# Kernel tuning notes

Hardware: AMD Instinct MI355X
Metric: run time of the kernel (lower is better)

Reference implementation:

```python
import jax, jax.numpy as jnp
import numpy as np

D = 64       # CNF state dimension
H = 512      # MLP hidden width
B = 8192     # batch


def setup_inputs() -> dict:
    key = jax.random.key(0)
    ks = jax.random.split(key, 8)
    s1 = 1.0 / np.sqrt(D + 1)
    s2 = 1.0 / np.sqrt(H)
    return {
        "t": jax.random.uniform(ks[0], (1,), dtype=jnp.float32),
        "x": jax.random.normal(ks[1], (B, D + 1), dtype=jnp.float32),
        "W1": jax.random.normal(ks[2], (D + 1, H), dtype=jnp.float32) * s1,
        "b1": jnp.zeros((H,), dtype=jnp.float32),
        "W2": jax.random.normal(ks[3], (H, H), dtype=jnp.float32) * s2,
        "b2": jnp.zeros((H,), dtype=jnp.float32),
        "W3": jax.random.normal(ks[4], (H, D), dtype=jnp.float32) * s2,
        "b3": jnp.zeros((D,), dtype=jnp.float32),
    }


def reference(t, x, W1, b1, W2, b2, W3, b3):
    # CNF.forward: strip log-density channel, evaluate vf and its exact divergence.
    xs = x[..., :-1]                      # [B, D]
    tt = t[0]

    def vf_single(xi):                    # xi: [D] -> [D]
        inp = jnp.concatenate([tt[None], xi])          # vf(t*ones, x) with t prepended
        h = jnp.tanh(inp @ W1 + b1)
        h = jnp.tanh(h @ W2 + b2)
        return h @ W3 + b3

    dx = jax.vmap(vf_single)(xs)                        # [B, D]
    # exact divergence: trace of per-sample Jacobian via reverse-mode (matches torch jacrev)
    J = jax.vmap(jax.jacrev(vf_single))(xs)             # [B, D, D]
    div = jnp.trace(J, axis1=-2, axis2=-1)              # [B]
    return jnp.concatenate([dx, div[:, None]], axis=-1) # [B, D+1]
```

## Files before the change

kernel.cpp:

```cpp
#include <hip/hip_runtime.h>

#define HH 512
#define DD 64
#define MROWS 32
#define TPB 1024
#define LP 520

typedef unsigned short u16;
typedef short s16x8 __attribute__((ext_vector_type(8)));
typedef float f32x4 __attribute__((ext_vector_type(4)));

#define MFMA16(A,B,C) __builtin_amdgcn_mfma_f32_16x16x32_bf16((A),(B),(C),0,0,0)

#define OFF_EF   0
#define OFF_W2F  (HH*HH)
#define OFF_W1F  (2*HH*HH)
#define OFF_W3F  (2*HH*HH + HH*DD)
#define OFF_Z0B  ((2*HH*HH + 2*HH*DD)*2)

__device__ __forceinline__ u16 f2bf(float f) {
    unsigned u = __builtin_bit_cast(unsigned, f);
    u += 0x7fffu + ((u >> 16) & 1u);
    return (u16)(u >> 16);
}
__device__ __forceinline__ float bf2f(u16 h) {
    return __builtin_bit_cast(float, (unsigned)h << 16);
}
__device__ __forceinline__ float fast_tanh(float x) {
    float e = __expf(2.0f * x);
    return 1.0f - 2.0f * __builtin_amdgcn_rcpf(e + 1.0f);
}

__global__ __launch_bounds__(256) void precompute(
    const float* __restrict__ t,  const float* __restrict__ W1,
    const float* __restrict__ b1, const float* __restrict__ W2,
    const float* __restrict__ W3, u16* __restrict__ ws16, float* __restrict__ z0)
{
    __shared__ float GL[16 * 520];
    u16* Ef  = ws16 + OFF_EF;
    u16* W2f = ws16 + OFF_W2F;
    u16* W1f = ws16 + OFF_W1F;
    u16* W3f = ws16 + OFF_W3F;

    const int bid = blockIdx.x, tid = threadIdx.x;

    if (bid < 32) {
        const int nt   = bid;
        const int a0   = nt * 16;
        const int lane = tid & 63, w = tid >> 6;
        const int m16  = lane & 15, q = lane >> 4;

        s16x8 afh[2], afl[2];
#pragma unroll
        for (int h = 0; h < 2; ++h) {
#pragma unroll
            for (int j = 0; j < 8; ++j) {
                int i = h * 32 + q * 8 + j;
                float v = W1[(1 + i) * HH + a0 + m16];
                u16 hi = f2bf(v);
                afh[h][j] = (short)hi;
                afl[h][j] = (short)f2bf(v - bf2f(hi));
            }
        }
        for (int bt = 0; bt < 8; ++bt) {
            int b0 = w * 128 + bt * 16;
            s16x8 bfh[2], bfl[2];
#pragma unroll
            for (int h = 0; h < 2; ++h) {
                const float* src = W3 + (b0 + m16) * DD + h * 32 + q * 8;
                float4 p0 = *(const float4*)(src);
                float4 p1 = *(const float4*)(src + 4);
                float vv[8] = {p0.x,p0.y,p0.z,p0.w,p1.x,p1.y,p1.z,p1.w};
#pragma unroll
                for (int j = 0; j < 8; ++j) {
                    u16 hi = f2bf(vv[j]);
                    bfh[h][j] = (short)hi;
                    bfl[h][j] = (short)f2bf(vv[j] - bf2f(hi));
                }
            }
            f32x4 c = {0.f, 0.f, 0.f, 0.f};
#pragma unroll
            for (int h = 0; h < 2; ++h) {
                c = MFMA16(afh[h], bfh[h], c);
                c = MFMA16(afh[h], bfl[h], c);
                c = MFMA16(afl[h], bfh[h], c);
            }
#pragma unroll
            for (int r = 0; r < 4; ++r)
                GL[(4 * q + r) * 520 + b0 + m16] = c[r];
        }
        __syncthreads();

        for (int p = 0; p < 4; ++p) {
            int ks = p * 4 + (tid >> 6);
            int ln = tid & 63;
            int al = ln & 15;
            int bq = ks * 32 + (ln >> 4) * 8;
            const float* w2p = W2 + (a0 + al) * HH + bq;
            const float* glp = GL + al * 520 + bq;
            float4 wa = *(const float4*)(w2p), wb = *(const float4*)(w2p + 4);
            float4 ga = *(const float4*)(glp), gb = *(const float4*)(glp + 4);
            s16x8 o;
            o[0]=(short)f2bf(wa.x*ga.x); o[1]=(short)f2bf(wa.y*ga.y);
            o[2]=(short)f2bf(wa.z*ga.z); o[3]=(short)f2bf(wa.w*ga.w);
            o[4]=(short)f2bf(wb.x*gb.x); o[5]=(short)f2bf(wb.y*gb.y);
            o[6]=(short)f2bf(wb.z*gb.z); o[7]=(short)f2bf(wb.w*gb.w);
            *(s16x8*)(Ef + nt * 8192 + ks * 512 + ln * 8) = o;
        }
        for (int p = 0; p < 4; ++p) {
            int ks = p * 4 + (tid >> 6);
            int ln = tid & 63;
            int n  = nt * 16 + (ln & 15);
            int k0 = ks * 32 + (ln >> 4) * 8;
            s16x8 o;
#pragma unroll
            for (int j = 0; j < 8; ++j) o[j] = (short)f2bf(W2[(k0 + j) * HH + n]);
            *(s16x8*)(W2f + nt * 8192 + ks * 512 + ln * 8) = o;
        }
        if (tid < 128) {
            int ks = tid >> 6, ln = tid & 63;
            int n  = nt * 16 + (ln & 15);
            int k0 = ks * 32 + (ln >> 4) * 8;
            s16x8 o;
#pragma unroll
            for (int j = 0; j < 8; ++j) o[j] = (short)f2bf(W1[(1 + k0 + j) * HH + n]);
            *(s16x8*)(W1f + nt * 1024 + ks * 512 + ln * 8) = o;
        }
    } else if (bid < 36) {
        int ot = bid - 32;
        for (int p = 0; p < 4; ++p) {
            int ks = p * 4 + (tid >> 6);
            int ln = tid & 63;
            int o  = ot * 16 + (ln & 15);
            int k0 = ks * 32 + (ln >> 4) * 8;
            s16x8 v;
#pragma unroll
            for (int j = 0; j < 8; ++j) v[j] = (short)f2bf(W3[(k0 + j) * DD + o]);
            *(s16x8*)(W3f + ot * 8192 + ks * 512 + ln * 8) = v;
        }
    } else {
        for (int n = tid; n < HH; n += 256)
            z0[n] = b1[n] + t[0] * W1[n];
    }
}

__global__ __launch_bounds__(TPB) void cnf_main(
    const float* __restrict__ x,  const u16* __restrict__ ws16,
    const float* __restrict__ z0, const float* __restrict__ b2,
    const float* __restrict__ b3, float* __restrict__ out)
{
    __shared__ u16 h1s[MROWS * LP];
    __shared__ u16 h2s[MROWS * LP];
    __shared__ u16 d2s[MROWS * LP];
    __shared__ float z0s[HH];
    __shared__ float b2s[HH];
    __shared__ float b3s[DD];
    __shared__ float divacc[16][MROWS];

    const u16* Ef  = ws16 + OFF_EF;
    const u16* W2f = ws16 + OFF_W2F;
    const u16* W1f = ws16 + OFF_W1F;
    const u16* W3f = ws16 + OFF_W3F;

    const int tid  = threadIdx.x;
    const int lane = tid & 63;
    const int w    = tid >> 6;
    const int m16  = lane & 15;
    const int q    = lane >> 4;
    const int kq   = q * 8;
    const int n1   = w * 32;
    const int r0   = blockIdx.x * MROWS;

    u16* xs = d2s;

    for (int idx = tid; idx < MROWS * DD; idx += TPB) {
        int r = idx >> 6, c = idx & 63;
        xs[r * 72 + c] = f2bf(x[(r0 + r) * (DD + 1) + c]);
    }
    if (tid < HH) { z0s[tid] = z0[tid]; b2s[tid] = b2[tid]; }
    if (tid < DD) b3s[tid] = b3[tid];
    __syncthreads();

    float d1reg[2][2][4];

    {
        s16x8 xa[2][2];
#pragma unroll
        for (int rt = 0; rt < 2; ++rt)
#pragma unroll
            for (int h = 0; h < 2; ++h)
                xa[rt][h] = *(const s16x8*)(xs + (rt * 16 + m16) * 72 + h * 32 + kq);
#pragma unroll
        for (int ct = 0; ct < 2; ++ct) {
            int nt = w * 2 + ct;
            s16x8 bw0 = *(const s16x8*)(W1f + nt * 1024 + lane * 8);
            s16x8 bw1 = *(const s16x8*)(W1f + nt * 1024 + 512 + lane * 8);
            int col = n1 + ct * 16 + m16;
#pragma unroll
            for (int rt = 0; rt < 2; ++rt) {
                f32x4 c = {0.f, 0.f, 0.f, 0.f};
                c = MFMA16(xa[rt][0], bw0, c);
                c = MFMA16(xa[rt][1], bw1, c);
#pragma unroll
                for (int i = 0; i < 4; ++i) {
                    float hv = fast_tanh(c[i] + z0s[col]);
                    h1s[(rt * 16 + 4 * q + i) * LP + col] = f2bf(hv);
                    d1reg[rt][ct][i] = 1.0f - hv * hv;
                }
            }
        }
    }
    __syncthreads();

    {
        f32x4 a00={0,0,0,0}, a01={0,0,0,0}, a10={0,0,0,0}, a11={0,0,0,0};
        const u16* ap0 = h1s + m16 * LP + kq;
        const u16* ap1 = h1s + (16 + m16) * LP + kq;
        const u16* bp0 = W2f + (2 * w + 0) * 8192 + lane * 8;
        const u16* bp1 = W2f + (2 * w + 1) * 8192 + lane * 8;
        s16x8 bA0 = *(const s16x8*)(bp0);
        s16x8 bA1 = *(const s16x8*)(bp1);
        s16x8 bB0 = *(const s16x8*)(bp0 + 512);
        s16x8 bB1 = *(const s16x8*)(bp1 + 512);
#pragma unroll 2
        for (int ks = 0; ks < 16; ks += 2) {
            int k2 = (ks + 2) & 15, k3 = (ks + 3) & 15;
            s16x8 nA0 = *(const s16x8*)(bp0 + k2 * 512);
            s16x8 nA1 = *(const s16x8*)(bp1 + k2 * 512);
            s16x8 f0  = *(const s16x8*)(ap0 + ks * 32);
            s16x8 f1  = *(const s16x8*)(ap1 + ks * 32);
            a00 = MFMA16(f0, bA0, a00);
            a10 = MFMA16(f1, bA0, a10);
            a01 = MFMA16(f0, bA1, a01);
            a11 = MFMA16(f1, bA1, a11);
            s16x8 nB0 = *(const s16x8*)(bp0 + k3 * 512);
            s16x8 nB1 = *(const s16x8*)(bp1 + k3 * 512);
            s16x8 f2  = *(const s16x8*)(ap0 + ks * 32 + 32);
            s16x8 f3  = *(const s16x8*)(ap1 + ks * 32 + 32);
            a00 = MFMA16(f2, bB0, a00);
            a10 = MFMA16(f3, bB0, a10);
            a01 = MFMA16(f2, bB1, a01);
            a11 = MFMA16(f3, bB1, a11);
            bA0 = nA0; bA1 = nA1; bB0 = nB0; bB1 = nB1;
        }
        f32x4 acc[2][2] = {{a00, a01}, {a10, a11}};
#pragma unroll
        for (int rt = 0; rt < 2; ++rt)
#pragma unroll
            for (int ct = 0; ct < 2; ++ct) {
                int col = n1 + ct * 16 + m16;
#pragma unroll
                for (int i = 0; i < 4; ++i) {
                    int row = rt * 16 + 4 * q + i;
                    float hv = fast_tanh(acc[rt][ct][i] + b2s[col]);
                    h2s[row * LP + col] = f2bf(hv);
                    d2s[row * LP + col] = f2bf(1.0f - hv * hv);
                }
            }
    }
    __syncthreads();

    if (w < 8) {
        const int rowt = w >> 2, ot = w & 3;
        f32x4 c3 = {0.f, 0.f, 0.f, 0.f};
        const u16* ap = h2s + (rowt * 16 + m16) * LP + kq;
        const u16* bp = W3f + ot * 8192 + lane * 8;
#pragma unroll 4
        for (int ks = 0; ks < 16; ++ks)
            c3 = MFMA16(*(const s16x8*)(ap + ks * 32),
                        *(const s16x8*)(bp + ks * 512), c3);
        int o = ot * 16 + m16;
#pragma unroll
        for (int i = 0; i < 4; ++i)
            out[(r0 + rowt * 16 + 4 * q + i) * (DD + 1) + o] = c3[i] + b3s[o];
    }

    {
        f32x4 a00={0,0,0,0}, a01={0,0,0,0}, a10={0,0,0,0}, a11={0,0,0,0};
        const u16* ap0 = d2s + m16 * LP + kq;
        const u16* ap1 = d2s + (16 + m16) * LP + kq;
        const u16* bp0 = Ef + (2 * w + 0) * 8192 + lane * 8;
        const u16* bp1 = Ef + (2 * w + 1) * 8192 + lane * 8;
        s16x8 bA0 = *(const s16x8*)(bp0);
        s16x8 bA1 = *(const s16x8*)(bp1);
        s16x8 bB0 = *(const s16x8*)(bp0 + 512);
        s16x8 bB1 = *(const s16x8*)(bp1 + 512);
#pragma unroll 2
        for (int ks = 0; ks < 16; ks += 2) {
            int k2 = (ks + 2) & 15, k3 = (ks + 3) & 15;
            s16x8 nA0 = *(const s16x8*)(bp0 + k2 * 512);
            s16x8 nA1 = *(const s16x8*)(bp1 + k2 * 512);
            s16x8 f0  = *(const s16x8*)(ap0 + ks * 32);
            s16x8 f1  = *(const s16x8*)(ap1 + ks * 32);
            a00 = MFMA16(f0, bA0, a00);
            a10 = MFMA16(f1, bA0, a10);
            a01 = MFMA16(f0, bA1, a01);
            a11 = MFMA16(f1, bA1, a11);
            s16x8 nB0 = *(const s16x8*)(bp0 + k3 * 512);
            s16x8 nB1 = *(const s16x8*)(bp1 + k3 * 512);
            s16x8 f2  = *(const s16x8*)(ap0 + ks * 32 + 32);
            s16x8 f3  = *(const s16x8*)(ap1 + ks * 32 + 32);
            a00 = MFMA16(f2, bB0, a00);
            a10 = MFMA16(f3, bB0, a10);
            a01 = MFMA16(f2, bB1, a01);
            a11 = MFMA16(f3, bB1, a11);
            bA0 = nA0; bA1 = nA1; bB0 = nB0; bB1 = nB1;
        }
        f32x4 acc[2][2] = {{a00, a01}, {a10, a11}};
#pragma unroll
        for (int rt = 0; rt < 2; ++rt)
#pragma unroll
            for (int i = 0; i < 4; ++i) {
                float v = d1reg[rt][0][i] * acc[rt][0][i]
                        + d1reg[rt][1][i] * acc[rt][1][i];
                v += __shfl_xor(v, 1, 64);
                v += __shfl_xor(v, 2, 64);
                v += __shfl_xor(v, 4, 64);
                v += __shfl_xor(v, 8, 64);
                if (m16 == 0) divacc[w][rt * 16 + 4 * q + i] = v;
            }
    }
    __syncthreads();

    if (tid < MROWS) {
        float s = 0.0f;
#pragma unroll
        for (int ww = 0; ww < 16; ++ww) s += divacc[ww][tid];
        out[(r0 + tid) * (DD + 1) + DD] = s;
    }
}

extern "C" void kernel_launch(void* const* d_in, const int* in_sizes, int n_in,
                              void* d_out, int out_size, void* d_ws, size_t ws_size,
                              hipStream_t stream) {
    const float* t  = (const float*)d_in[0];
    const float* x  = (const float*)d_in[1];
    const float* W1 = (const float*)d_in[2];
    const float* b1 = (const float*)d_in[3];
    const float* W2 = (const float*)d_in[4];
    const float* b2 = (const float*)d_in[5];
    const float* W3 = (const float*)d_in[6];
    const float* b3 = (const float*)d_in[7];
    float* out = (float*)d_out;

    u16*   ws16 = (u16*)d_ws;
    float* z0   = (float*)((char*)d_ws + OFF_Z0B);

    precompute<<<37, 256, 0, stream>>>(t, W1, b1, W2, W3, ws16, z0);
    cnf_main<<<8192 / MROWS, TPB, 0, stream>>>(x, ws16, z0, b2, b3, out);
}
```

Before: 97.95 us.

## Split precompute across more blocks and hoist weight-fragment loads in main kernel

The precompute kernel grows from 37 to 137 blocks, splitting each Ef/W2f/W3f tile over two half-K blocks. The W2 and W3 transposes are now staged through shared memory with coalesced float4 loads instead of strided scalar reads. In the main kernel, the W1 fragments and the first W2 fragments are loaded before the x staging loop so their global latency overlaps that work, at the cost of more live registers at kernel start.

```diff
diff --git a/kernel.cpp b/kernel.cpp
--- a/kernel.cpp
+++ b/kernel.cpp
@@ -36,23 +36,23 @@
     const float* __restrict__ b1, const float* __restrict__ W2,
     const float* __restrict__ W3, u16* __restrict__ ws16, float* __restrict__ z0)
 {
-    __shared__ float GL[16 * 520];
+    __shared__ float T[16 * 264 > 256 * 20 ? 16 * 264 : 256 * 20];
     u16* Ef  = ws16 + OFF_EF;
     u16* W2f = ws16 + OFF_W2F;
     u16* W1f = ws16 + OFF_W1F;
     u16* W3f = ws16 + OFF_W3F;
 
     const int bid = blockIdx.x, tid = threadIdx.x;
-
-    if (bid < 32) {
-        const int nt   = bid;
-        const int a0   = nt * 16;
-        const int lane = tid & 63, w = tid >> 6;
-        const int m16  = lane & 15, q = lane >> 4;
+    const int lane = tid & 63, wv = tid >> 6;
+    const int m16 = lane & 15, q = lane >> 4;
+
+    if (bid < 64) {
+        const int nt = bid >> 1, bh = bid & 1;
+        const int a0 = nt * 16, b0 = bh * 256;
 
         s16x8 afh[2], afl[2];
 #pragma unroll
-        for (int h = 0; h < 2; ++h) {
+        for (int h = 0; h < 2; ++h)
 #pragma unroll
             for (int j = 0; j < 8; ++j) {
                 int i = h * 32 + q * 8 + j;
@@ -61,13 +61,13 @@
                 afh[h][j] = (short)hi;
                 afl[h][j] = (short)f2bf(v - bf2f(hi));
             }
-        }
-        for (int bt = 0; bt < 8; ++bt) {
-            int b0 = w * 128 + bt * 16;
+#pragma unroll
+        for (int bt = 0; bt < 4; ++bt) {
+            int bl = wv * 64 + bt * 16;
             s16x8 bfh[2], bfl[2];
 #pragma unroll
             for (int h = 0; h < 2; ++h) {
-                const float* src = W3 + (b0 + m16) * DD + h * 32 + q * 8;
+                const float* src = W3 + (b0 + bl + m16) * DD + h * 32 + q * 8;
                 float4 p0 = *(const float4*)(src);
                 float4 p1 = *(const float4*)(src + 4);
                 float vv[8] = {p0.x,p0.y,p0.z,p0.w,p1.x,p1.y,p1.z,p1.w};
@@ -87,37 +87,26 @@
             }
 #pragma unroll
             for (int r = 0; r < 4; ++r)
-                GL[(4 * q + r) * 520 + b0 + m16] = c[r];
+                T[(4 * q + r) * 264 + bl + m16] = c[r];
         }
         __syncthreads();
 
-        for (int p = 0; p < 4; ++p) {
-            int ks = p * 4 + (tid >> 6);
-            int ln = tid & 63;
-            int al = ln & 15;
-            int bq = ks * 32 + (ln >> 4) * 8;
-            const float* w2p = W2 + (a0 + al) * HH + bq;
-            const float* glp = GL + al * 520 + bq;
+#pragma unroll
+        for (int p = 0; p < 2; ++p) {
+            int ksl = p * 4 + wv;
+            int al  = m16;
+            int blc = ksl * 32 + q * 8;
+            const float* w2p = W2 + (a0 + al) * HH + b0 + blc;
             float4 wa = *(const float4*)(w2p), wb = *(const float4*)(w2p + 4);
-            float4 ga = *(const float4*)(glp), gb = *(const float4*)(glp + 4);
+            const float* glp = T + al * 264 + blc;
             s16x8 o;
-            o[0]=(short)f2bf(wa.x*ga.x); o[1]=(short)f2bf(wa.y*ga.y);
-            o[2]=(short)f2bf(wa.z*ga.z); o[3]=(short)f2bf(wa.w*ga.w);
-            o[4]=(short)f2bf(wb.x*gb.x); o[5]=(short)f2bf(wb.y*gb.y);
-            o[6]=(short)f2bf(wb.z*gb.z); o[7]=(short)f2bf(wb.w*gb.w);
-            *(s16x8*)(Ef + nt * 8192 + ks * 512 + ln * 8) = o;
-        }
-        for (int p = 0; p < 4; ++p) {
-            int ks = p * 4 + (tid >> 6);
-            int ln = tid & 63;
-            int n  = nt * 16 + (ln & 15);
-            int k0 = ks * 32 + (ln >> 4) * 8;
-            s16x8 o;
-#pragma unroll
-            for (int j = 0; j < 8; ++j) o[j] = (short)f2bf(W2[(k0 + j) * HH + n]);
-            *(s16x8*)(W2f + nt * 8192 + ks * 512 + ln * 8) = o;
-        }
-        if (tid < 128) {
+            o[0]=(short)f2bf(wa.x*glp[0]); o[1]=(short)f2bf(wa.y*glp[1]);
+            o[2]=(short)f2bf(wa.z*glp[2]); o[3]=(short)f2bf(wa.w*glp[3]);
+            o[4]=(short)f2bf(wb.x*glp[4]); o[5]=(short)f2bf(wb.y*glp[5]);
+            o[6]=(short)f2bf(wb.z*glp[6]); o[7]=(short)f2bf(wb.w*glp[7]);
+            *(s16x8*)(Ef + nt * 8192 + (b0 / 32 + ksl) * 512 + lane * 8) = o;
+        }
+        if (bh == 0 && tid < 128) {
             int ks = tid >> 6, ln = tid & 63;
             int n  = nt * 16 + (ln & 15);
             int k0 = ks * 32 + (ln >> 4) * 8;
@@ -126,17 +115,45 @@
             for (int j = 0; j < 8; ++j) o[j] = (short)f2bf(W1[(1 + k0 + j) * HH + n]);
             *(s16x8*)(W1f + nt * 1024 + ks * 512 + ln * 8) = o;
         }
-    } else if (bid < 36) {
-        int ot = bid - 32;
-        for (int p = 0; p < 4; ++p) {
-            int ks = p * 4 + (tid >> 6);
-            int ln = tid & 63;
-            int o  = ot * 16 + (ln & 15);
-            int k0 = ks * 32 + (ln >> 4) * 8;
-            s16x8 v;
-#pragma unroll
-            for (int j = 0; j < 8; ++j) v[j] = (short)f2bf(W3[(k0 + j) * DD + o]);
-            *(s16x8*)(W3f + ot * 8192 + ks * 512 + ln * 8) = v;
+    } else if (bid < 128) {
+        const int nt = (bid - 64) >> 1, kh = (bid - 64) & 1;
+        const int n0 = nt * 16, k0 = kh * 256;
+#pragma unroll
+        for (int it = 0; it < 4; ++it) {
+            int r = (tid >> 2) + it * 64;
+            int c = (tid & 3) * 4;
+            float4 v = *(const float4*)(W2 + (k0 + r) * HH + n0 + c);
+            *(float4*)(T + r * 20 + c) = v;
+        }
+        __syncthreads();
+#pragma unroll
+        for (int p = 0; p < 2; ++p) {
+            int ksl = p * 4 + wv;
+            int kq  = ksl * 32 + q * 8;
+            s16x8 o;
+#pragma unroll
+            for (int j = 0; j < 8; ++j) o[j] = (short)f2bf(T[(kq + j) * 20 + m16]);
+            *(s16x8*)(W2f + nt * 8192 + (k0 / 32 + ksl) * 512 + lane * 8) = o;
+        }
+    } else if (bid < 136) {
+        const int ot = (bid - 128) >> 1, kh = (bid - 128) & 1;
+        const int o0 = ot * 16, k0 = kh * 256;
+#pragma unroll
+        for (int it = 0; it < 4; ++it) {
+            int r = (tid >> 2) + it * 64;
+            int c = (tid & 3) * 4;
+            float4 v = *(const float4*)(W3 + (k0 + r) * DD + o0 + c);
+            *(float4*)(T + r * 20 + c) = v;
+        }
+        __syncthreads();
+#pragma unroll
+        for (int p = 0; p < 2; ++p) {
+            int ksl = p * 4 + wv;
+            int kq  = ksl * 32 + q * 8;
+            s16x8 o;
+#pragma unroll
+            for (int j = 0; j < 8; ++j) o[j] = (short)f2bf(T[(kq + j) * 20 + m16]);
+            *(s16x8*)(W3f + ot * 8192 + (k0 / 32 + ksl) * 512 + lane * 8) = o;
         }
     } else {
         for (int n = tid; n < HH; n += 256)
@@ -173,6 +190,20 @@
 
     u16* xs = d2s;
 
+    s16x8 p1b[2][2];
+#pragma unroll
+    for (int ct = 0; ct < 2; ++ct) {
+        const u16* bb = W1f + (w * 2 + ct) * 1024 + lane * 8;
+        p1b[ct][0] = *(const s16x8*)(bb);
+        p1b[ct][1] = *(const s16x8*)(bb + 512);
+    }
+    const u16* w2bp0 = W2f + (2 * w + 0) * 8192 + lane * 8;
+    const u16* w2bp1 = W2f + (2 * w + 1) * 8192 + lane * 8;
+    s16x8 bA0 = *(const s16x8*)(w2bp0);
+    s16x8 bA1 = *(const s16x8*)(w2bp1);
+    s16x8 bB0 = *(const s16x8*)(w2bp0 + 512);
+    s16x8 bB1 = *(const s16x8*)(w2bp1 + 512);
+
     for (int idx = tid; idx < MROWS * DD; idx += TPB) {
         int r = idx >> 6, c = idx & 63;
         xs[r * 72 + c] = f2bf(x[(r0 + r) * (DD + 1) + c]);
@@ -192,15 +223,12 @@
                 xa[rt][h] = *(const s16x8*)(xs + (rt * 16 + m16) * 72 + h * 32 + kq);
 #pragma unroll
         for (int ct = 0; ct < 2; ++ct) {
-            int nt = w * 2 + ct;
-            s16x8 bw0 = *(const s16x8*)(W1f + nt * 1024 + lane * 8);
-            s16x8 bw1 = *(const s16x8*)(W1f + nt * 1024 + 512 + lane * 8);
             int col = n1 + ct * 16 + m16;
 #pragma unroll
             for (int rt = 0; rt < 2; ++rt) {
                 f32x4 c = {0.f, 0.f, 0.f, 0.f};
-                c = MFMA16(xa[rt][0], bw0, c);
-                c = MFMA16(xa[rt][1], bw1, c);
+                c = MFMA16(xa[rt][0], p1b[ct][0], c);
+                c = MFMA16(xa[rt][1], p1b[ct][1], c);
 #pragma unroll
                 for (int i = 0; i < 4; ++i) {
                     float hv = fast_tanh(c[i] + z0s[col]);
@@ -216,25 +244,19 @@
         f32x4 a00={0,0,0,0}, a01={0,0,0,0}, a10={0,0,0,0}, a11={0,0,0,0};
         const u16* ap0 = h1s + m16 * LP + kq;
         const u16* ap1 = h1s + (16 + m16) * LP + kq;
-        const u16* bp0 = W2f + (2 * w + 0) * 8192 + lane * 8;
-        const u16* bp1 = W2f + (2 * w + 1) * 8192 + lane * 8;
-        s16x8 bA0 = *(const s16x8*)(bp0);
-        s16x8 bA1 = *(const s16x8*)(bp1);
-        s16x8 bB0 = *(const s16x8*)(bp0 + 512);
-        s16x8 bB1 = *(const s16x8*)(bp1 + 512);
 #pragma unroll 2
         for (int ks = 0; ks < 16; ks += 2) {
             int k2 = (ks + 2) & 15, k3 = (ks + 3) & 15;
-            s16x8 nA0 = *(const s16x8*)(bp0 + k2 * 512);
-            s16x8 nA1 = *(const s16x8*)(bp1 + k2 * 512);
+            s16x8 nA0 = *(const s16x8*)(w2bp0 + k2 * 512);
+            s16x8 nA1 = *(const s16x8*)(w2bp1 + k2 * 512);
             s16x8 f0  = *(const s16x8*)(ap0 + ks * 32);
             s16x8 f1  = *(const s16x8*)(ap1 + ks * 32);
             a00 = MFMA16(f0, bA0, a00);
             a10 = MFMA16(f1, bA0, a10);
             a01 = MFMA16(f0, bA1, a01);
             a11 = MFMA16(f1, bA1, a11);
-            s16x8 nB0 = *(const s16x8*)(bp0 + k3 * 512);
-            s16x8 nB1 = *(const s16x8*)(bp1 + k3 * 512);
+            s16x8 nB0 = *(const s16x8*)(w2bp0 + k3 * 512);
+            s16x8 nB1 = *(const s16x8*)(w2bp1 + k3 * 512);
             s16x8 f2  = *(const s16x8*)(ap0 + ks * 32 + 32);
             s16x8 f3  = *(const s16x8*)(ap1 + ks * 32 + 32);
             a00 = MFMA16(f2, bB0, a00);
@@ -281,10 +303,10 @@
         const u16* ap1 = d2s + (16 + m16) * LP + kq;
         const u16* bp0 = Ef + (2 * w + 0) * 8192 + lane * 8;
         const u16* bp1 = Ef + (2 * w + 1) * 8192 + lane * 8;
-        s16x8 bA0 = *(const s16x8*)(bp0);
-        s16x8 bA1 = *(const s16x8*)(bp1);
-        s16x8 bB0 = *(const s16x8*)(bp0 + 512);
-        s16x8 bB1 = *(const s16x8*)(bp1 + 512);
+        s16x8 cA0 = *(const s16x8*)(bp0);
+        s16x8 cA1 = *(const s16x8*)(bp1);
+        s16x8 cB0 = *(const s16x8*)(bp0 + 512);
+        s16x8 cB1 = *(const s16x8*)(bp1 + 512);
 #pragma unroll 2
         for (int ks = 0; ks < 16; ks += 2) {
             int k2 = (ks + 2) & 15, k3 = (ks + 3) & 15;
@@ -292,19 +314,19 @@
             s16x8 nA1 = *(const s16x8*)(bp1 + k2 * 512);
             s16x8 f0  = *(const s16x8*)(ap0 + ks * 32);
             s16x8 f1  = *(const s16x8*)(ap1 + ks * 32);
-            a00 = MFMA16(f0, bA0, a00);
-            a10 = MFMA16(f1, bA0, a10);
-            a01 = MFMA16(f0, bA1, a01);
-            a11 = MFMA16(f1, bA1, a11);
+            a00 = MFMA16(f0, cA0, a00);
+            a10 = MFMA16(f1, cA0, a10);
+            a01 = MFMA16(f0, cA1, a01);
+            a11 = MFMA16(f1, cA1, a11);
             s16x8 nB0 = *(const s16x8*)(bp0 + k3 * 512);
             s16x8 nB1 = *(const s16x8*)(bp1 + k3 * 512);
             s16x8 f2  = *(const s16x8*)(ap0 + ks * 32 + 32);
             s16x8 f3  = *(const s16x8*)(ap1 + ks * 32 + 32);
-            a00 = MFMA16(f2, bB0, a00);
-            a10 = MFMA16(f3, bB0, a10);
-            a01 = MFMA16(f2, bB1, a01);
-            a11 = MFMA16(f3, bB1, a11);
-            bA0 = nA0; bA1 = nA1; bB0 = nB0; bB1 = nB1;
+            a00 = MFMA16(f2, cB0, a00);
+            a10 = MFMA16(f3, cB0, a10);
+            a01 = MFMA16(f2, cB1, a01);
+            a11 = MFMA16(f3, cB1, a11);
+            cA0 = nA0; cA1 = nA1; cB0 = nB0; cB1 = nB1;
         }
         f32x4 acc[2][2] = {{a00, a01}, {a10, a11}};
 #pragma unroll
@@ -346,6 +368,6 @@
     u16*   ws16 = (u16*)d_ws;
     float* z0   = (float*)((char*)d_ws + OFF_Z0B);
 
-    precompute<<<37, 256, 0, stream>>>(t, W1, b1, W2, W3, ws16, z0);
+    precompute<<<137, 256, 0, stream>>>(t, W1, b1, W2, W3, ws16, z0);
     cnf_main<<<8192 / MROWS, TPB, 0, stream>>>(x, ws16, z0, b2, b3, out);
 }
```

Result: faster. 94.94 us (-3.1%).
